# Kernel optimization log

Hardware: AMD Instinct MI355X
Metric: run time of the kernel (lower is better)

The kernel has to match this reference:

```python
import jax, jax.numpy as jnp
import numpy as np

N = 100000      # total nodes = B_GRAPHS * NODES_PER_GRAPH
NPG = 1000      # nodes per graph (num_nodes in module)
B_GRAPHS = 100
H = 128         # hidden_channels
CIN = 3         # in_channels
E = 1600000     # edges (avg_degree 16)
OUT = 2         # out_channels


def setup_inputs() -> dict:
    key = jax.random.key(0)
    ks = jax.random.split(key, 20)
    s = 0.05
    inp = {
        "x": jax.random.normal(ks[0], (N, CIN), jnp.float32),
        "edge_index": jnp.stack([
            jax.random.randint(ks[1], (E,), 0, N),
            jax.random.randint(ks[2], (E,), 0, N),
        ]).astype(jnp.int64),
        "batch": jnp.repeat(jnp.arange(B_GRAPHS), NPG).astype(jnp.int64),
        # DiffusionConv layer 0: CIN -> H ; layer 1: H -> H
        "W_self0": jax.random.normal(ks[3], (CIN, H), jnp.float32) * s,
        "W_nbr0": jax.random.normal(ks[4], (CIN, H), jnp.float32) * s,
        "b0": jnp.zeros((H,), jnp.float32),
        "W_self1": jax.random.normal(ks[5], (H, H), jnp.float32) * s,
        "W_nbr1": jax.random.normal(ks[6], (H, H), jnp.float32) * s,
        "b1": jnp.zeros((H,), jnp.float32),
        # 2 stacked LSTMs (torch layout: W_ih [4H, in], W_hh [4H, H])
        "Wih0": jax.random.normal(ks[7], (4 * H, H), jnp.float32) * s,
        "Whh0": jax.random.normal(ks[8], (4 * H, H), jnp.float32) * s,
        "bih0": jnp.zeros((4 * H,), jnp.float32),
        "bhh0": jnp.zeros((4 * H,), jnp.float32),
        "Wih1": jax.random.normal(ks[9], (4 * H, H), jnp.float32) * s,
        "Whh1": jax.random.normal(ks[10], (4 * H, H), jnp.float32) * s,
        "bih1": jnp.zeros((4 * H,), jnp.float32),
        "bhh1": jnp.zeros((4 * H,), jnp.float32),
        # output head
        "W_out": jax.random.normal(ks[11], (H, OUT), jnp.float32) * s,
        "b_out": jnp.zeros((OUT,), jnp.float32),
    }
    return inp


def diffusion_conv(h, src, dst, W_self, W_nbr, b):
    # gather-aggregate-transform: out = h W_self + (D^-1 A h) W_nbr + b
    msgs = h[src]                                            # [E, C] gather
    agg = jax.ops.segment_sum(msgs, dst, num_segments=N)     # [N, C] scatter-add
    deg = jax.ops.segment_sum(jnp.ones((src.shape[0], 1), h.dtype), dst,
                              num_segments=N)                # [N, 1]
    agg = agg / jnp.maximum(deg, 1.0)
    return h @ W_self + agg @ W_nbr + b


def lstm_layer(x_seq, Wih, Whh, bih, bhh):
    # x_seq: [T, Bn, H] seq-first, zero initial state (torch default)
    Bn = x_seq.shape[1]
    h0 = jnp.zeros((Bn, H), x_seq.dtype)
    c0 = jnp.zeros((Bn, H), x_seq.dtype)

    def step(carry, xt):
        h, c = carry
        g = xt @ Wih.T + h @ Whh.T + (bih + bhh)   # [Bn, 4H]
        i, f, gg, o = jnp.split(g, 4, axis=-1)     # torch gate order i,f,g,o
        c = jax.nn.sigmoid(f) * c + jax.nn.sigmoid(i) * jnp.tanh(gg)
        h = jax.nn.sigmoid(o) * jnp.tanh(c)
        return (h, c), h

    _, hs = jax.lax.scan(step, (h0, c0), x_seq)
    return hs


def reference(x, edge_index, batch, W_self0, W_nbr0, b0, W_self1, W_nbr1, b1,
              Wih0, Whh0, bih0, bhh0, Wih1, Whh1, bih1, bhh1, W_out, b_out):
    src, dst = edge_index[0], edge_index[1]
    h = jax.nn.relu(diffusion_conv(x, src, dst, W_self0, W_nbr0, b0))
    h = jax.nn.relu(diffusion_conv(h, src, dst, W_self1, W_nbr1, b1))
    # view(-1, num_nodes, hidden): [B_GRAPHS, NPG, H], LSTM seq-first
    seq = h.reshape(B_GRAPHS, NPG, H)
    seq = lstm_layer(seq, Wih0, Whh0, bih0, bhh0)
    seq = lstm_layer(seq, Wih1, Whh1, bih1, bhh1)
    h = seq.reshape(N, H)
    # global_mean_pool over batch vector
    pooled = jax.ops.segment_sum(h, batch, num_segments=B_GRAPHS)
    cnt = jax.ops.segment_sum(jnp.ones((N, 1), h.dtype), batch,
                              num_segments=B_GRAPHS)
    pooled = pooled / jnp.maximum(cnt, 1.0)
    logits = pooled @ W_out + b_out                # [B_GRAPHS, OUT]
    return jax.nn.log_softmax(logits, axis=1)
```

## Files before the change

kernel.cpp:

```cpp
#include <hip/hip_runtime.h>

#define N_NODES 100000
#define NPG     1000
#define B_GR    100
#define HDIM    128
#define E_EDGES 1600000

typedef __attribute__((ext_vector_type(8))) short bf16x8;
typedef __attribute__((ext_vector_type(4))) float f32x4;
typedef unsigned long long u64;
typedef unsigned short u16;

__device__ __forceinline__ float sigf(float x) { return 1.f / (1.f + __expf(-x)); }
__device__ __forceinline__ float tanh_fast(float x) { return 1.f - 2.f / (__expf(2.f * x) + 1.f); }
__device__ __forceinline__ u16 f2bf(float f) {
    unsigned u = __float_as_uint(f);
    unsigned r = (u + 0x7fffu + ((u >> 16) & 1u)) >> 16;
    return (u16)r;
}
__device__ __forceinline__ float bf2f(u16 h) { return __uint_as_float(((unsigned)h) << 16); }
__device__ __forceinline__ f32x4 MF(bf16x8 a, bf16x8 b, f32x4 c) {
    return __builtin_amdgcn_mfma_f32_16x16x32_bf16(a, b, c, 0, 0, 0);
}
#define BAR() asm volatile("s_waitcnt lgkmcnt(0)\n\ts_barrier" ::: "memory")

__global__ void k_count(const int* __restrict__ dst, int* __restrict__ cnt) {
    int e = blockIdx.x * 256 + threadIdx.x;
    if (e < E_EDGES) atomicAdd(&cnt[dst[e]], 1);
}

__global__ void k_scan1(const int* __restrict__ cnt, int* __restrict__ row_ptr, int* __restrict__ bsum) {
    __shared__ int sd[256];
    int tid = threadIdx.x;
    int base = blockIdx.x * 1024 + tid * 4;
    int v[4];
#pragma unroll
    for (int j = 0; j < 4; ++j) {
        int i = base + j;
        v[j] = (i < N_NODES) ? cnt[i] : 0;
    }
    int s = v[0] + v[1] + v[2] + v[3];
    sd[tid] = s;
    __syncthreads();
    for (int off = 1; off < 256; off <<= 1) {
        int t = (tid >= off) ? sd[tid - off] : 0;
        __syncthreads();
        sd[tid] += t;
        __syncthreads();
    }
    int excl = sd[tid] - s;
    int run = excl;
#pragma unroll
    for (int j = 0; j < 4; ++j) {
        int i = base + j;
        run += v[j];
        if (i < N_NODES) row_ptr[1 + i] = run;
    }
    if (tid == 255) bsum[blockIdx.x] = sd[255];
}

__global__ void k_scan2(int* __restrict__ bsum, int nb) {
    if (threadIdx.x == 0 && blockIdx.x == 0) {
        int carry = 0;
        for (int b = 0; b < nb; ++b) {
            int t = bsum[b];
            bsum[b] = carry;
            carry += t;
        }
    }
}

__global__ void k_scan3(int* __restrict__ row_ptr, const int* __restrict__ bsum, int* __restrict__ cursor) {
    int i = blockIdx.x * 256 + threadIdx.x;
    if (i >= N_NODES) return;
    int incl = row_ptr[1 + i] + bsum[i >> 10];
    row_ptr[1 + i] = incl;
    if (i == 0) { row_ptr[0] = 0; cursor[0] = 0; }
    if (i + 1 < N_NODES) cursor[i + 1] = incl;
}

__global__ void k_fill(const int* __restrict__ src, const int* __restrict__ dst,
                       int* __restrict__ cursor, int* __restrict__ csr_src) {
    int e = blockIdx.x * 256 + threadIdx.x;
    if (e >= E_EDGES) return;
    int d = dst[e];
    int pos = atomicAdd(&cursor[d], 1);
    csr_src[pos] = src[e];
}

__global__ void k_conv0(const float* __restrict__ x, const int* __restrict__ rp, const int* __restrict__ csr,
                        const float* __restrict__ Ws, const float* __restrict__ Wn, const float* __restrict__ b,
                        u16* __restrict__ Hbf) {
    int n = blockIdx.x;
    int tid = threadIdx.x;
    __shared__ float sagg[3];
    if (tid < 3) sagg[tid] = 0.f;
    __syncthreads();
    int s0 = rp[n], s1 = rp[n + 1];
    int deg = s1 - s0;
    for (int j = tid; j < deg; j += 128) {
        int s = csr[s0 + j];
        atomicAdd(&sagg[0], x[s * 3 + 0]);
        atomicAdd(&sagg[1], x[s * 3 + 1]);
        atomicAdd(&sagg[2], x[s * 3 + 2]);
    }
    __syncthreads();
    float inv = 1.f / fmaxf((float)deg, 1.f);
    float a0 = sagg[0] * inv, a1 = sagg[1] * inv, a2 = sagg[2] * inv;
    float x0 = x[n * 3 + 0], x1 = x[n * 3 + 1], x2 = x[n * 3 + 2];
    float acc = b[tid]
        + x0 * Ws[0 * 128 + tid] + x1 * Ws[1 * 128 + tid] + x2 * Ws[2 * 128 + tid]
        + a0 * Wn[0 * 128 + tid] + a1 * Wn[1 * 128 + tid] + a2 * Wn[2 * 128 + tid];
    Hbf[(size_t)n * 128 + tid] = f2bf(fmaxf(acc, 0.f));
}

__global__ __launch_bounds__(256)
void k_agg2(const u16* __restrict__ hin, const int* __restrict__ rp, const int* __restrict__ csr,
            float* __restrict__ out) {
    int wid = threadIdx.x >> 6;
    int l = threadIdx.x & 63;
    int n = blockIdx.x * 4 + wid;
    if (n >= N_NODES) return;
    int s0 = rp[n], deg = rp[n + 1] - s0;
    float ax = 0.f, ay = 0.f;
    const unsigned* base = (const unsigned*)hin;
    for (int c0 = 0; c0 < deg; c0 += 64) {
        int m = min(64, deg - c0);
        int myidx = csr[s0 + c0 + ((l < m) ? l : 0)];
        int j = 0;
        for (; j + 4 <= m; j += 4) {
            int i0 = __shfl(myidx, j);
            int i1 = __shfl(myidx, j + 1);
            int i2 = __shfl(myidx, j + 2);
            int i3 = __shfl(myidx, j + 3);
            unsigned v0 = base[(size_t)i0 * 64 + l];
            unsigned v1 = base[(size_t)i1 * 64 + l];
            unsigned v2 = base[(size_t)i2 * 64 + l];
            unsigned v3 = base[(size_t)i3 * 64 + l];
            ax += bf2f((u16)v0); ay += bf2f((u16)(v0 >> 16));
            ax += bf2f((u16)v1); ay += bf2f((u16)(v1 >> 16));
            ax += bf2f((u16)v2); ay += bf2f((u16)(v2 >> 16));
            ax += bf2f((u16)v3); ay += bf2f((u16)(v3 >> 16));
        }
        for (; j < m; ++j) {
            int i0 = __shfl(myidx, j);
            unsigned v = base[(size_t)i0 * 64 + l];
            ax += bf2f((u16)v); ay += bf2f((u16)(v >> 16));
        }
    }
    float dv = fmaxf((float)deg, 1.f);
    float2 o; o.x = ax / dv; o.y = ay / dv;
    *(float2*)&out[(size_t)n * 128 + l * 2] = o;
}

__global__ __launch_bounds__(256)
void k_conv1mm(const u16* __restrict__ Hbf, float* __restrict__ B,
               const float* __restrict__ Wself, const float* __restrict__ Wnbr,
               const float* __restrict__ bias) {
    __shared__ float As[64 * 64];
    __shared__ float Wls[64 * 128];
    int tid = threadIdx.x;
    int r0 = blockIdx.x * 64;
    int tx = tid & 31, ty = tid >> 5;
    float acc[8][4];
#pragma unroll
    for (int r = 0; r < 8; ++r)
#pragma unroll
        for (int j = 0; j < 4; ++j) acc[r][j] = 0.f;

    for (int chunk = 0; chunk < 4; ++chunk) {
        const float* Wsrc = (chunk < 2) ? Wself : Wnbr;
        int k0 = (chunk & 1) * 64;
#pragma unroll
        for (int i = 0; i < 4; ++i) {
            int e = tid + 256 * i;
            int row = e >> 4, c4 = e & 15;
            int grow = r0 + row;
            float4 v = make_float4(0.f, 0.f, 0.f, 0.f);
            if (grow < N_NODES) {
                if (chunk < 2) {
                    u64 p = *(const u64*)&Hbf[(size_t)grow * 128 + k0 + c4 * 4];
                    v.x = bf2f((u16)p);         v.y = bf2f((u16)(p >> 16));
                    v.z = bf2f((u16)(p >> 32)); v.w = bf2f((u16)(p >> 48));
                } else {
                    v = *(const float4*)&B[(size_t)grow * 128 + k0 + c4 * 4];
                }
            }
            *(float4*)&As[row * 64 + c4 * 4] = v;
        }
#pragma unroll
        for (int i = 0; i < 8; ++i) {
            int e = tid + 256 * i;
            int row = e >> 5, c4 = e & 31;
            *(float4*)&Wls[row * 128 + c4 * 4] = *(const float4*)&Wsrc[(k0 + row) * 128 + c4 * 4];
        }
        __syncthreads();
#pragma unroll 4
        for (int kk = 0; kk < 64; ++kk) {
            float4 w = *(const float4*)&Wls[kk * 128 + tx * 4];
#pragma unroll
            for (int r = 0; r < 8; ++r) {
                float a = As[(ty + 8 * r) * 64 + kk];
                acc[r][0] += a * w.x; acc[r][1] += a * w.y;
                acc[r][2] += a * w.z; acc[r][3] += a * w.w;
            }
        }
        __syncthreads();
    }
    float4 bb = *(const float4*)&bias[tx * 4];
#pragma unroll
    for (int r = 0; r < 8; ++r) {
        int grow = r0 + ty + 8 * r;
        if (grow < N_NODES) {
            float4 v;
            v.x = fmaxf(acc[r][0] + bb.x, 0.f);
            v.y = fmaxf(acc[r][1] + bb.y, 0.f);
            v.z = fmaxf(acc[r][2] + bb.z, 0.f);
            v.w = fmaxf(acc[r][3] + bb.w, 0.f);
            *(float4*)&B[grow * 128 + tx * 4] = v;
        }
    }
}

__global__ void k_tobf16(const float* __restrict__ C, u16* __restrict__ Xf) {
    int g = blockIdx.x * 256 + threadIdx.x;
    int vr = g >> 5;
    int c4 = g & 31;
    int t = vr / 1008;
    int rv = vr - t * 1008;
    int r = min(rv, NPG - 1);
    int n = t * NPG + r;
    int col0 = c4 * 4;
    f32x4 v = *(const f32x4*)(C + (size_t)n * 128 + col0);
    u16 h0 = f2bf(v[0]), h1 = f2bf(v[1]), h2 = f2bf(v[2]), h3 = f2bf(v[3]);
    u64 pk = (u64)h0 | ((u64)h1 << 16) | ((u64)h2 << 32) | ((u64)h3 << 48);
    int rb = rv >> 4, rr = rv & 15;
    size_t idx = (size_t)(t * 63 + rb) * 2048
               + (size_t)((col0 >> 5) * 512 + ((col0 >> 3) & 3) * 128 + rr * 8 + (col0 & 7));
    *(u64*)(Xf + idx) = pk;
}

__global__ void k_prepf(const float* __restrict__ Wih0, const float* __restrict__ Whh0,
                        const float* __restrict__ Wih1, const float* __restrict__ Whh1,
                        u16* __restrict__ WTf) {
    int idx = blockIdx.x * 256 + threadIdx.x;
    int lane = idx & 63;
    int gt = (idx >> 6) & 3;
    int kt = (idx >> 8) & 7;
    int w  = (idx >> 11) & 7;
    int l  = idx >> 14;
    int d = 16 * w + (lane & 15);
    int k0 = kt * 32 + (lane >> 4) * 8;
    int wrow = gt * 128 + d;
    const float* Wi = l ? Wih1 : Wih0;
    const float* Wh = l ? Whh1 : Whh0;
    const float* srcp = (k0 < 128) ? (Wi + wrow * 128 + k0) : (Wh + wrow * 128 + (k0 - 128));
    u16 o[8];
#pragma unroll
    for (int j = 0; j < 8; ++j) o[j] = f2bf(srcp[j]);
    u64* dst = (u64*)(WTf + (size_t)idx * 8);
    dst[0] = (u64)o[0] | ((u64)o[1] << 16) | ((u64)o[2] << 32) | ((u64)o[3] << 48);
    dst[1] = (u64)o[4] | ((u64)o[5] << 16) | ((u64)o[6] << 32) | ((u64)o[7] << 48);
}

__global__ void k_bsum(const float* __restrict__ bih0, const float* __restrict__ bhh0,
                       const float* __restrict__ bih1, const float* __restrict__ bhh1,
                       float* __restrict__ bs) {
    int i = blockIdx.x * 256 + threadIdx.x;
    int l = i >> 9, c = i & 511;
    bs[i] = l ? (bih1[c] + bhh1[c]) : (bih0[c] + bhh0[c]);
}

#define LSTM_STEP(ACC, ACCN, T, CUR)                                                   \
    do {                                                                               \
        BAR();                                                                         \
        _Pragma("unroll")                                                              \
        for (int kt = 0; kt < 4; ++kt) {                                               \
            bf16x8 af = *(const bf16x8*)(hsh[CUR] + kt * 512 + l * 8);                 \
            ACC[0] = MF(af, Bw[4 + kt][0], ACC[0]);                                    \
            ACC[1] = MF(af, Bw[4 + kt][1], ACC[1]);                                    \
            ACC[2] = MF(af, Bw[4 + kt][2], ACC[2]);                                    \
            ACC[3] = MF(af, Bw[4 + kt][3], ACC[3]);                                    \
        }                                                                              \
        if (mode == 0 && (T) > 0)                                                      \
            ((u64*)(Hout + (size_t)(((T) - 1) * 63 + rb) * 2048))[tid] =               \
                ((const u64*)hsh[CUR])[tid];                                           \
        if ((T) < 99) {                                                                \
            _Pragma("unroll")                                                          \
            for (int g = 0; g < 4; ++g) ACCN[g] = (f32x4){0.f, 0.f, 0.f, 0.f};         \
            _Pragma("unroll")                                                          \
            for (int kt = 0; kt < 4; ++kt) {                                           \
                ACCN[0] = MF(xf[kt], Bw[kt][0], ACCN[0]);                              \
                ACCN[1] = MF(xf[kt], Bw[kt][1], ACCN[1]);                              \
                ACCN[2] = MF(xf[kt], Bw[kt][2], ACCN[2]);                              \
                ACCN[3] = MF(xf[kt], Bw[kt][3], ACCN[3]);                              \
            }                                                                          \
        }                                                                              \
        if ((T) < 98) {                                                                \
            const u16* xn = xbase + (size_t)((T) + 2) * TSTR;                          \
            _Pragma("unroll")                                                          \
            for (int kt = 0; kt < 4; ++kt)                                             \
                xf[kt] = *(const bf16x8*)(xn + kt * 512);                              \
        }                                                                              \
        float hsum = 0.f;                                                              \
        _Pragma("unroll")                                                              \
        for (int reg = 0; reg < 4; ++reg) {                                            \
            float gi = ACC[0][reg] + bi;                                               \
            float gf = ACC[1][reg] + bf_;                                              \
            float gg = ACC[2][reg] + bg;                                               \
            float go = ACC[3][reg] + bo;                                               \
            float cprev = (reg == 0) ? cst0 : (reg == 1) ? cst1 : (reg == 2) ? cst2 : cst3; \
            float c = sigf(gf) * cprev + sigf(gi) * tanh_fast(gg);                     \
            if (reg == 0) cst0 = c; else if (reg == 1) cst1 = c;                       \
            else if (reg == 2) cst2 = c; else cst3 = c;                                \
            float h = sigf(go) * tanh_fast(c);                                         \
            hsh[(CUR) ^ 1][hbase + reg * 8] = f2bf(h);                                 \
            if (mode == 1) {                                                           \
                int row = (l >> 4) * 4 + reg;                                          \
                if (row < nreal) hsum += h;                                            \
            }                                                                          \
        }                                                                              \
        if (mode == 1) {                                                               \
            hsum += __shfl_xor(hsum, 16);                                              \
            hsum += __shfl_xor(hsum, 32);                                              \
            if ((l >> 4) == 0) atomicAdd(&pooled[(T) * 128 + d], hsum);                \
        }                                                                              \
    } while (0)

__global__ __launch_bounds__(512, 1)
void k_lstm_layer(const u16* __restrict__ Xf, const u16* __restrict__ WTl,
                  const float* __restrict__ bsL, u16* __restrict__ Hout,
                  float* __restrict__ pooled, int mode) {
    __shared__ __align__(16) u16 hsh[2][2048];
    int tid = threadIdx.x;
    int l = tid & 63;
    int w = tid >> 6;
    int rb = blockIdx.x;
    int n0 = rb * 16;
    int nreal = min(16, NPG - n0);

    bf16x8 Bw[8][4];
    const bf16x8* Wv = (const bf16x8*)WTl;
#pragma unroll
    for (int kt = 0; kt < 8; ++kt)
#pragma unroll
        for (int gt = 0; gt < 4; ++gt)
            Bw[kt][gt] = Wv[((w * 8 + kt) * 4 + gt) * 64 + l];

    int d = (w << 4) | (l & 15);
    float bi = bsL[d], bf_ = bsL[128 + d], bg = bsL[256 + d], bo = bsL[384 + d];
    float cst0 = 0.f, cst1 = 0.f, cst2 = 0.f, cst3 = 0.f;

    int ktp = d >> 5, oct = (d >> 3) & 3, boff = d & 7;
    int hbase = ktp * 512 + ((l >> 4) * 4 + 16 * oct) * 8 + boff;

    const u16* xbase = Xf + (size_t)rb * 2048 + l * 8;
    const size_t TSTR = (size_t)63 * 2048;

    bf16x8 xf[4];
#pragma unroll
    for (int kt = 0; kt < 4; ++kt) xf[kt] = *(const bf16x8*)(xbase + kt * 512);

    f32x4 accA[4], accB[4];
#pragma unroll
    for (int g = 0; g < 4; ++g) accA[g] = (f32x4){0.f, 0.f, 0.f, 0.f};
#pragma unroll
    for (int kt = 0; kt < 4; ++kt) {
        accA[0] = MF(xf[kt], Bw[kt][0], accA[0]);
        accA[1] = MF(xf[kt], Bw[kt][1], accA[1]);
        accA[2] = MF(xf[kt], Bw[kt][2], accA[2]);
        accA[3] = MF(xf[kt], Bw[kt][3], accA[3]);
    }
#pragma unroll
    for (int kt = 0; kt < 4; ++kt) xf[kt] = *(const bf16x8*)(xbase + TSTR + kt * 512);

    ((u64*)hsh[0])[tid] = 0ull;

    for (int t2 = 0; t2 < 50; ++t2) {
        int t0 = 2 * t2;
        LSTM_STEP(accA, accB, t0, 0);
        LSTM_STEP(accB, accA, t0 + 1, 1);
    }
    BAR();
    if (mode == 0)
        ((u64*)(Hout + (size_t)(99 * 63 + rb) * 2048))[tid] = ((const u64*)hsh[0])[tid];
}

__global__ void k_head(const float* __restrict__ pooled, const float* __restrict__ Wout,
                       const float* __restrict__ bout, float* __restrict__ out) {
    int gi = threadIdx.x;
    if (gi >= B_GR) return;
    float l0 = bout[0], l1 = bout[1];
    for (int d = 0; d < 128; ++d) {
        float p = pooled[gi * 128 + d] / 1000.0f;
        l0 += p * Wout[d * 2 + 0];
        l1 += p * Wout[d * 2 + 1];
    }
    float m = fmaxf(l0, l1);
    float lse = m + logf(__expf(l0 - m) + __expf(l1 - m));
    out[gi * 2 + 0] = l0 - lse;
    out[gi * 2 + 1] = l1 - lse;
}

extern "C" void kernel_launch(void* const* d_in, const int* in_sizes, int n_in,
                              void* d_out, int out_size, void* d_ws, size_t ws_size,
                              hipStream_t stream) {
    const float* x    = (const float*)d_in[0];
    const int*   ei   = (const int*)d_in[1];
    const int*   srcI = ei;
    const int*   dstI = ei + E_EDGES;
    const float* Ws0  = (const float*)d_in[3];
    const float* Wn0  = (const float*)d_in[4];
    const float* b0   = (const float*)d_in[5];
    const float* Ws1  = (const float*)d_in[6];
    const float* Wn1  = (const float*)d_in[7];
    const float* b1   = (const float*)d_in[8];
    const float* Wih0 = (const float*)d_in[9];
    const float* Whh0 = (const float*)d_in[10];
    const float* bih0 = (const float*)d_in[11];
    const float* bhh0 = (const float*)d_in[12];
    const float* Wih1 = (const float*)d_in[13];
    const float* Whh1 = (const float*)d_in[14];
    const float* bih1 = (const float*)d_in[15];
    const float* bhh1 = (const float*)d_in[16];
    const float* Wout = (const float*)d_in[17];
    const float* bout = (const float*)d_in[18];
    float* out = (float*)d_out;

    char* ws = (char*)d_ws;
    int*   row_ptr = (int*)(ws + 0);
    int*   cursor  = (int*)(ws + 400128);
    int*   csr_src = (int*)(ws + 800128);
    int*   bsum    = (int*)(ws + 7200128);
    u16*   Hbf     = (u16*)(ws + 7200640);
    float* bufB    = (float*)(ws + 58400640);
    u16*   WTf     = (u16*)(ws + 109600640);
    float* bsB     = (float*)(ws + 110649216);
    float* pooled  = (float*)(ws + 110653312);

    u16* Xf  = (u16*)(ws + 7200640);
    u16* H0f = (u16*)(ws + 33005440);

    hipMemsetAsync(cursor, 0, N_NODES * sizeof(int), stream);
    hipMemsetAsync(pooled, 0, B_GR * 128 * sizeof(float), stream);

    k_count<<<E_EDGES / 256, 256, 0, stream>>>(dstI, cursor);
    k_scan1<<<98, 256, 0, stream>>>(cursor, row_ptr, bsum);
    k_scan2<<<1, 64, 0, stream>>>(bsum, 98);
    k_scan3<<<(N_NODES + 255) / 256, 256, 0, stream>>>(row_ptr, bsum, cursor);
    k_fill<<<E_EDGES / 256, 256, 0, stream>>>(srcI, dstI, cursor, csr_src);

    k_conv0<<<N_NODES, 128, 0, stream>>>(x, row_ptr, csr_src, Ws0, Wn0, b0, Hbf);
    k_agg2<<<N_NODES / 4, 256, 0, stream>>>(Hbf, row_ptr, csr_src, bufB);
    k_conv1mm<<<(N_NODES + 63) / 64, 256, 0, stream>>>(Hbf, bufB, Ws1, Wn1, b1);
    k_tobf16<<<12600, 256, 0, stream>>>(bufB, Xf);

    k_prepf<<<128, 256, 0, stream>>>(Wih0, Whh0, Wih1, Whh1, WTf);
    k_bsum<<<4, 256, 0, stream>>>(bih0, bhh0, bih1, bhh1, bsB);

    k_lstm_layer<<<63, 512, 0, stream>>>(Xf, WTf, bsB, H0f, nullptr, 0);
    k_lstm_layer<<<63, 512, 0, stream>>>(H0f, WTf + 131072, bsB + 512, nullptr, pooled, 1);

    k_head<<<1, 128, 0, stream>>>(pooled, Wout, bout, out);
}
```

Before: 838.3 us.

## Split LSTM into parallel input-GEMM and recurrent kernels with LDS-resident weights

The fused per-layer LSTM kernel is replaced by two kernels. The first precomputes the input projection plus bias for 50 timesteps at once across 315 blocks and stores it as bf16. The second runs only the recurrent h·Whh product with weights held in LDS, carrying h and c state between halves through global memory. This takes the input GEMM off the serial critical path and frees registers that held the weights. In exchange it adds extra launches and global round-trips for the gate preactivations, and rounds those preactivations to bf16.

```diff
diff --git a/kernel.cpp b/kernel.cpp
--- a/kernel.cpp
+++ b/kernel.cpp
@@ -22,7 +22,10 @@
 __device__ __forceinline__ f32x4 MF(bf16x8 a, bf16x8 b, f32x4 c) {
     return __builtin_amdgcn_mfma_f32_16x16x32_bf16(a, b, c, 0, 0, 0);
 }
-#define BAR() asm volatile("s_waitcnt lgkmcnt(0)\n\ts_barrier" ::: "memory")
+__device__ __forceinline__ u64 pack4(f32x4 a) {
+    return (u64)f2bf(a[0]) | ((u64)f2bf(a[1]) << 16)
+         | ((u64)f2bf(a[2]) << 32) | ((u64)f2bf(a[3]) << 48);
+}
 
 __global__ void k_count(const int* __restrict__ dst, int* __restrict__ cnt) {
     int e = blockIdx.x * 256 + threadIdx.x;
@@ -271,119 +274,160 @@
     bs[i] = l ? (bih1[c] + bhh1[c]) : (bih0[c] + bhh0[c]);
 }
 
-#define LSTM_STEP(ACC, ACCN, T, CUR)                                                   \
-    do {                                                                               \
-        BAR();                                                                         \
-        _Pragma("unroll")                                                              \
-        for (int kt = 0; kt < 4; ++kt) {                                               \
-            bf16x8 af = *(const bf16x8*)(hsh[CUR] + kt * 512 + l * 8);                 \
-            ACC[0] = MF(af, Bw[4 + kt][0], ACC[0]);                                    \
-            ACC[1] = MF(af, Bw[4 + kt][1], ACC[1]);                                    \
-            ACC[2] = MF(af, Bw[4 + kt][2], ACC[2]);                                    \
-            ACC[3] = MF(af, Bw[4 + kt][3], ACC[3]);                                    \
-        }                                                                              \
-        if (mode == 0 && (T) > 0)                                                      \
-            ((u64*)(Hout + (size_t)(((T) - 1) * 63 + rb) * 2048))[tid] =               \
-                ((const u64*)hsh[CUR])[tid];                                           \
-        if ((T) < 99) {                                                                \
-            _Pragma("unroll")                                                          \
-            for (int g = 0; g < 4; ++g) ACCN[g] = (f32x4){0.f, 0.f, 0.f, 0.f};         \
-            _Pragma("unroll")                                                          \
-            for (int kt = 0; kt < 4; ++kt) {                                           \
-                ACCN[0] = MF(xf[kt], Bw[kt][0], ACCN[0]);                              \
-                ACCN[1] = MF(xf[kt], Bw[kt][1], ACCN[1]);                              \
-                ACCN[2] = MF(xf[kt], Bw[kt][2], ACCN[2]);                              \
-                ACCN[3] = MF(xf[kt], Bw[kt][3], ACCN[3]);                              \
-            }                                                                          \
-        }                                                                              \
-        if ((T) < 98) {                                                                \
-            const u16* xn = xbase + (size_t)((T) + 2) * TSTR;                          \
-            _Pragma("unroll")                                                          \
-            for (int kt = 0; kt < 4; ++kt)                                             \
-                xf[kt] = *(const bf16x8*)(xn + kt * 512);                              \
-        }                                                                              \
-        float hsum = 0.f;                                                              \
-        _Pragma("unroll")                                                              \
-        for (int reg = 0; reg < 4; ++reg) {                                            \
-            float gi = ACC[0][reg] + bi;                                               \
-            float gf = ACC[1][reg] + bf_;                                              \
-            float gg = ACC[2][reg] + bg;                                               \
-            float go = ACC[3][reg] + bo;                                               \
-            float cprev = (reg == 0) ? cst0 : (reg == 1) ? cst1 : (reg == 2) ? cst2 : cst3; \
-            float c = sigf(gf) * cprev + sigf(gi) * tanh_fast(gg);                     \
-            if (reg == 0) cst0 = c; else if (reg == 1) cst1 = c;                       \
-            else if (reg == 2) cst2 = c; else cst3 = c;                                \
-            float h = sigf(go) * tanh_fast(c);                                         \
-            hsh[(CUR) ^ 1][hbase + reg * 8] = f2bf(h);                                 \
-            if (mode == 1) {                                                           \
-                int row = (l >> 4) * 4 + reg;                                          \
-                if (row < nreal) hsum += h;                                            \
-            }                                                                          \
-        }                                                                              \
-        if (mode == 1) {                                                               \
-            hsum += __shfl_xor(hsum, 16);                                              \
-            hsum += __shfl_xor(hsum, 32);                                              \
-            if ((l >> 4) == 0) atomicAdd(&pooled[(T) * 128 + d], hsum);                \
-        }                                                                              \
-    } while (0)
-
 __global__ __launch_bounds__(512, 1)
-void k_lstm_layer(const u16* __restrict__ Xf, const u16* __restrict__ WTl,
-                  const float* __restrict__ bsL, u16* __restrict__ Hout,
-                  float* __restrict__ pooled, int mode) {
-    __shared__ __align__(16) u16 hsh[2][2048];
+void k_gemmA(const u16* __restrict__ src, const u16* __restrict__ WTf,
+             const float* __restrict__ bsB, u16* __restrict__ Gx, int t0, int layer) {
+    extern __shared__ __align__(16) u16 smem[];
     int tid = threadIdx.x;
-    int l = tid & 63;
-    int w = tid >> 6;
+    int l = tid & 63, w = tid >> 6;
+    int rb = blockIdx.x % 63;
+    int slice = blockIdx.x / 63;
+    {
+        const u64* Wsrc = (const u64*)(WTf + (size_t)layer * 131072);
+        u64* Wd = (u64*)smem;
+#pragma unroll
+        for (int i = 0; i < 32; ++i) {
+            int j = tid + i * 512;
+            int dfrag = j >> 7, r = j & 127;
+            int w_ = dfrag >> 4, kt2 = (dfrag >> 2) & 3, gt = dfrag & 3;
+            int gfrag = (w_ * 8 + kt2) * 4 + gt;
+            Wd[j] = Wsrc[(size_t)gfrag * 128 + r];
+        }
+    }
+    __syncthreads();
+    int d = (w << 4) | (l & 15);
+    float b0v = bsB[layer * 512 + d];
+    float b1v = bsB[layer * 512 + 128 + d];
+    float b2v = bsB[layer * 512 + 256 + d];
+    float b3v = bsB[layer * 512 + 384 + d];
+    const u16* wbase = smem + (size_t)w * 8192 + l * 8;
+    for (int tt = 0; tt < 10; ++tt) {
+        int t = t0 + slice * 10 + tt;
+        const u16* xb = src + ((size_t)t * 63 + rb) * 2048 + l * 8;
+        bf16x8 x0 = *(const bf16x8*)(xb);
+        bf16x8 x1 = *(const bf16x8*)(xb + 512);
+        bf16x8 x2 = *(const bf16x8*)(xb + 1024);
+        bf16x8 x3 = *(const bf16x8*)(xb + 1536);
+        f32x4 a0 = {b0v, b0v, b0v, b0v};
+        f32x4 a1 = {b1v, b1v, b1v, b1v};
+        f32x4 a2 = {b2v, b2v, b2v, b2v};
+        f32x4 a3 = {b3v, b3v, b3v, b3v};
+#pragma unroll
+        for (int kt2 = 0; kt2 < 4; ++kt2) {
+            bf16x8 xa = (kt2 == 0) ? x0 : (kt2 == 1) ? x1 : (kt2 == 2) ? x2 : x3;
+            a0 = MF(xa, *(const bf16x8*)(wbase + (kt2 * 4 + 0) * 512), a0);
+            a1 = MF(xa, *(const bf16x8*)(wbase + (kt2 * 4 + 1) * 512), a1);
+            a2 = MF(xa, *(const bf16x8*)(wbase + (kt2 * 4 + 2) * 512), a2);
+            a3 = MF(xa, *(const bf16x8*)(wbase + (kt2 * 4 + 3) * 512), a3);
+        }
+        size_t gbase = ((size_t)(t - t0) * 63 + rb) * 8192 + (size_t)w * 1024 + l * 4;
+        *(u64*)(Gx + gbase)       = pack4(a0);
+        *(u64*)(Gx + gbase + 256) = pack4(a1);
+        *(u64*)(Gx + gbase + 512) = pack4(a2);
+        *(u64*)(Gx + gbase + 768) = pack4(a3);
+    }
+}
+
+__global__ __launch_bounds__(512, 1)
+void k_recB(const u16* __restrict__ Gx, const u16* __restrict__ WTf,
+            u16* __restrict__ H0f, float* __restrict__ pooled,
+            u16* __restrict__ hstate, float* __restrict__ cstate,
+            int t0, int layer) {
+    extern __shared__ __align__(16) u16 smem[];
+    u16* Wlds = smem;
+    u16* hshA = smem + 65536;
+    u16* hshB = smem + 67584;
+    int tid = threadIdx.x;
+    int l = tid & 63, w = tid >> 6;
     int rb = blockIdx.x;
+
+    {
+        u64 hv = (t0 == 0) ? 0ull : ((const u64*)(hstate + (size_t)rb * 2048))[tid];
+        ((u64*)hshA)[tid] = hv;
+    }
+    {
+        const u64* Wsrc = (const u64*)(WTf + (size_t)layer * 131072);
+        u64* Wd = (u64*)Wlds;
+#pragma unroll
+        for (int i = 0; i < 32; ++i) {
+            int j = tid + i * 512;
+            int dfrag = j >> 7, r = j & 127;
+            int w_ = dfrag >> 4, kt2 = (dfrag >> 2) & 3, gt = dfrag & 3;
+            int gfrag = (w_ * 8 + 4 + kt2) * 4 + gt;
+            Wd[j] = Wsrc[(size_t)gfrag * 128 + r];
+        }
+    }
+    float cst0, cst1, cst2, cst3;
+    if (t0 == 0) {
+        cst0 = cst1 = cst2 = cst3 = 0.f;
+    } else {
+        const f32x4 cv = *(const f32x4*)(cstate + ((size_t)rb * 512 + tid) * 4);
+        cst0 = cv[0]; cst1 = cv[1]; cst2 = cv[2]; cst3 = cv[3];
+    }
+    __syncthreads();
+
+    int d = (w << 4) | (l & 15);
+    int ktp = d >> 5, oct = (d >> 3) & 3, boff = d & 7;
+    int hbase = ktp * 512 + ((l >> 4) * 4 + 16 * oct) * 8 + boff;
+    const u16* wbase = Wlds + (size_t)w * 8192 + l * 8;
     int n0 = rb * 16;
     int nreal = min(16, NPG - n0);
-
-    bf16x8 Bw[8][4];
-    const bf16x8* Wv = (const bf16x8*)WTl;
-#pragma unroll
-    for (int kt = 0; kt < 8; ++kt)
-#pragma unroll
-        for (int gt = 0; gt < 4; ++gt)
-            Bw[kt][gt] = Wv[((w * 8 + kt) * 4 + gt) * 64 + l];
-
-    int d = (w << 4) | (l & 15);
-    float bi = bsL[d], bf_ = bsL[128 + d], bg = bsL[256 + d], bo = bsL[384 + d];
-    float cst0 = 0.f, cst1 = 0.f, cst2 = 0.f, cst3 = 0.f;
-
-    int ktp = d >> 5, oct = (d >> 3) & 3, boff = d & 7;
-    int hbase = ktp * 512 + ((l >> 4) * 4 + 16 * oct) * 8 + boff;
-
-    const u16* xbase = Xf + (size_t)rb * 2048 + l * 8;
-    const size_t TSTR = (size_t)63 * 2048;
-
-    bf16x8 xf[4];
-#pragma unroll
-    for (int kt = 0; kt < 4; ++kt) xf[kt] = *(const bf16x8*)(xbase + kt * 512);
-
-    f32x4 accA[4], accB[4];
-#pragma unroll
-    for (int g = 0; g < 4; ++g) accA[g] = (f32x4){0.f, 0.f, 0.f, 0.f};
-#pragma unroll
-    for (int kt = 0; kt < 4; ++kt) {
-        accA[0] = MF(xf[kt], Bw[kt][0], accA[0]);
-        accA[1] = MF(xf[kt], Bw[kt][1], accA[1]);
-        accA[2] = MF(xf[kt], Bw[kt][2], accA[2]);
-        accA[3] = MF(xf[kt], Bw[kt][3], accA[3]);
-    }
-#pragma unroll
-    for (int kt = 0; kt < 4; ++kt) xf[kt] = *(const bf16x8*)(xbase + TSTR + kt * 512);
-
-    ((u64*)hsh[0])[tid] = 0ull;
-
-    for (int t2 = 0; t2 < 50; ++t2) {
-        int t0 = 2 * t2;
-        LSTM_STEP(accA, accB, t0, 0);
-        LSTM_STEP(accB, accA, t0 + 1, 1);
-    }
-    BAR();
-    if (mode == 0)
-        ((u64*)(Hout + (size_t)(99 * 63 + rb) * 2048))[tid] = ((const u64*)hsh[0])[tid];
+    int cur = 0;
+
+    for (int tt = 0; tt < 50; ++tt) {
+        int t = t0 + tt;
+        size_t gbase = ((size_t)tt * 63 + rb) * 8192 + (size_t)w * 1024 + l * 4;
+        u64 p0 = *(const u64*)(Gx + gbase);
+        u64 p1 = *(const u64*)(Gx + gbase + 256);
+        u64 p2 = *(const u64*)(Gx + gbase + 512);
+        u64 p3 = *(const u64*)(Gx + gbase + 768);
+
+        const u16* hc = cur ? hshB : hshA;
+        u16* hn = cur ? hshA : hshB;
+        f32x4 a0 = {0.f, 0.f, 0.f, 0.f};
+        f32x4 a1 = {0.f, 0.f, 0.f, 0.f};
+        f32x4 a2 = {0.f, 0.f, 0.f, 0.f};
+        f32x4 a3 = {0.f, 0.f, 0.f, 0.f};
+#pragma unroll
+        for (int kt2 = 0; kt2 < 4; ++kt2) {
+            bf16x8 hf = *(const bf16x8*)(hc + kt2 * 512 + l * 8);
+            a0 = MF(hf, *(const bf16x8*)(wbase + (kt2 * 4 + 0) * 512), a0);
+            a1 = MF(hf, *(const bf16x8*)(wbase + (kt2 * 4 + 1) * 512), a1);
+            a2 = MF(hf, *(const bf16x8*)(wbase + (kt2 * 4 + 2) * 512), a2);
+            a3 = MF(hf, *(const bf16x8*)(wbase + (kt2 * 4 + 3) * 512), a3);
+        }
+        float hsum = 0.f;
+#pragma unroll
+        for (int reg = 0; reg < 4; ++reg) {
+            float gi = a0[reg] + bf2f((u16)(p0 >> (16 * reg)));
+            float gf = a1[reg] + bf2f((u16)(p1 >> (16 * reg)));
+            float gg = a2[reg] + bf2f((u16)(p2 >> (16 * reg)));
+            float go = a3[reg] + bf2f((u16)(p3 >> (16 * reg)));
+            float cprev = (reg == 0) ? cst0 : (reg == 1) ? cst1 : (reg == 2) ? cst2 : cst3;
+            float c = sigf(gf) * cprev + sigf(gi) * tanh_fast(gg);
+            if (reg == 0) cst0 = c; else if (reg == 1) cst1 = c;
+            else if (reg == 2) cst2 = c; else cst3 = c;
+            float h = sigf(go) * tanh_fast(c);
+            u16 hb = f2bf(h);
+            hn[hbase + reg * 8] = hb;
+            if (layer == 0) {
+                H0f[((size_t)t * 63 + rb) * 2048 + hbase + reg * 8] = hb;
+            } else {
+                int row = (l >> 4) * 4 + reg;
+                if (row < nreal) hsum += h;
+            }
+        }
+        if (layer == 1) {
+            hsum += __shfl_xor(hsum, 16);
+            hsum += __shfl_xor(hsum, 32);
+            if ((l >> 4) == 0) atomicAdd(&pooled[t * 128 + d], hsum);
+        }
+        __syncthreads();
+        cur ^= 1;
+    }
+    ((u64*)(hstate + (size_t)rb * 2048))[tid] = ((const u64*)(cur ? hshB : hshA))[tid];
+    f32x4 cv = {cst0, cst1, cst2, cst3};
+    *(f32x4*)(cstate + ((size_t)rb * 512 + tid) * 4) = cv;
 }
 
 __global__ void k_head(const float* __restrict__ pooled, const float* __restrict__ Wout,
@@ -433,13 +477,15 @@
     int*   csr_src = (int*)(ws + 800128);
     int*   bsum    = (int*)(ws + 7200128);
     u16*   Hbf     = (u16*)(ws + 7200640);
-    float* bufB    = (float*)(ws + 58400640);
-    u16*   WTf     = (u16*)(ws + 109600640);
-    float* bsB     = (float*)(ws + 110649216);
-    float* pooled  = (float*)(ws + 110653312);
-
-    u16* Xf  = (u16*)(ws + 7200640);
-    u16* H0f = (u16*)(ws + 33005440);
+    u16*   Xf      = (u16*)(ws + 7200640);
+    u16*   H0f     = (u16*)(ws + 33005440);
+    float* bufB    = (float*)(ws + 58810368);
+    u16*   Gx      = (u16*)(ws + 58810368);
+    u16*   WTf     = (u16*)(ws + 110419968);
+    float* bsB     = (float*)(ws + 110944256);
+    float* pooled  = (float*)(ws + 110948352);
+    u16*   hstate  = (u16*)(ws + 800128);
+    float* cstate  = (float*)(ws + 1058176);
 
     hipMemsetAsync(cursor, 0, N_NODES * sizeof(int), stream);
     hipMemsetAsync(pooled, 0, B_GR * 128 * sizeof(float), stream);
@@ -458,8 +504,17 @@
     k_prepf<<<128, 256, 0, stream>>>(Wih0, Whh0, Wih1, Whh1, WTf);
     k_bsum<<<4, 256, 0, stream>>>(bih0, bhh0, bih1, bhh1, bsB);
 
-    k_lstm_layer<<<63, 512, 0, stream>>>(Xf, WTf, bsB, H0f, nullptr, 0);
-    k_lstm_layer<<<63, 512, 0, stream>>>(H0f, WTf + 131072, bsB + 512, nullptr, pooled, 1);
+    hipFuncSetAttribute((const void*)k_gemmA, hipFuncAttributeMaxDynamicSharedMemorySize, 131072);
+    hipFuncSetAttribute((const void*)k_recB,  hipFuncAttributeMaxDynamicSharedMemorySize, 139264);
+
+    for (int layer = 0; layer < 2; ++layer) {
+        const u16* srcT = layer ? H0f : Xf;
+        for (int half = 0; half < 2; ++half) {
+            int t0 = half * 50;
+            k_gemmA<<<315, 512, 131072, stream>>>(srcT, WTf, bsB, Gx, t0, layer);
+            k_recB<<<63, 512, 139264, stream>>>(Gx, WTf, H0f, pooled, hstate, cstate, t0, layer);
+        }
+    }
 
     k_head<<<1, 128, 0, stream>>>(pooled, Wout, bout, out);
 }
```

After: 1.026 ms. +22.4%, slower.
